# Optimization experiments

Measured on AMD Instinct MI355X. Metric: run time of the kernel, lower is better.

Reference implementation:

```python
import jax, jax.numpy as jnp
import numpy as np

N_HEADS = 8
HEAD_CH = 64
NC = N_HEADS * HEAD_CH  # 512
SCALE = HEAD_CH ** -0.5


def _grid_sample_bilinear(img, grid):
    # img [N,C,H,W]; grid [N,Hg,Wg,2] as (x,y) in [-1,1]; align_corners=True, zeros padding
    N, C, H, W = img.shape
    gx, gy = grid[..., 0], grid[..., 1]
    ix = (gx + 1.0) * 0.5 * (W - 1)
    iy = (gy + 1.0) * 0.5 * (H - 1)
    ix0 = jnp.floor(ix)
    iy0 = jnp.floor(iy)
    ix1 = ix0 + 1.0
    iy1 = iy0 + 1.0
    flat = img.reshape(N, C, H * W)

    def gather(yy, xx):
        yi = jnp.clip(yy, 0, H - 1).astype(jnp.int32)
        xi = jnp.clip(xx, 0, W - 1).astype(jnp.int32)
        idx = (yi * W + xi).reshape(N, 1, -1)
        v = jnp.take_along_axis(flat, idx, axis=2)  # [N,C,Hg*Wg]
        m = ((yy >= 0) & (yy <= H - 1) & (xx >= 0) & (xx <= W - 1)).astype(img.dtype)
        return v * m.reshape(N, 1, -1)

    w00 = ((ix1 - ix) * (iy1 - iy)).reshape(N, 1, -1)
    w01 = ((ix - ix0) * (iy1 - iy)).reshape(N, 1, -1)
    w10 = ((ix1 - ix) * (iy - iy0)).reshape(N, 1, -1)
    w11 = ((ix - ix0) * (iy - iy0)).reshape(N, 1, -1)
    out = (gather(iy0, ix0) * w00 + gather(iy0, ix1) * w01 +
           gather(iy1, ix0) * w10 + gather(iy1, ix1) * w11)
    return out.reshape(N, C, grid.shape[1], grid.shape[2])


def _attn_single(qv, xv, w_q, b_q, w_k, b_k, w_v, b_v, w_o, b_o):
    # qv [Bx,C] single query; xv [Bx,C,L] keys/values; batched forward_attn_single
    Bx, L = qv.shape[0], xv.shape[2]
    qh = (qv @ w_q.T + b_q).reshape(Bx, N_HEADS, HEAD_CH)
    k = (jnp.einsum('oc,bcl->bol', w_k, xv) + b_k[None, :, None]).reshape(Bx, N_HEADS, HEAD_CH, L)
    v = (jnp.einsum('oc,bcl->bol', w_v, xv) + b_v[None, :, None]).reshape(Bx, N_HEADS, HEAD_CH, L)
    a = jax.nn.softmax(jnp.einsum('bhc,bhcl->bhl', qh, k) * SCALE, axis=-1)
    o = jnp.einsum('bhl,bhcl->bhc', a, v).reshape(Bx, NC)
    return o @ w_o.T + b_o


def _forward(q, x, w_off_proj, b_off_proj, w_dw, b_dw, ln_g, ln_b, w_off,
             w_q, b_q, w_k, b_k, w_v, b_v, w_o, b_o, H, W):
    B, NQ, C = q.shape
    x_img = x.transpose(0, 2, 1).reshape(B, C, H, W)
    # proj_offset (1x1 conv)
    t = jnp.einsum('oc,bchw->bohw', w_off_proj, x_img) + b_off_proj[None, :, None, None]
    # depthwise 3x3 conv (groups = channels), stride 1, pad 1
    t = jax.lax.conv_general_dilated(
        t, w_dw, (1, 1), ((1, 1), (1, 1)), feature_group_count=C,
        dimension_numbers=('NCHW', 'OIHW', 'NCHW')) + b_dw[None, :, None, None]
    # LayerNormProxy: LN over channel dim
    tc = t.transpose(0, 2, 3, 1)
    mu = tc.mean(-1, keepdims=True)
    var = tc.var(-1, keepdims=True)
    tc = (tc - mu) / jnp.sqrt(var + 1e-5) * ln_g + ln_b
    t = jax.nn.gelu(tc.transpose(0, 3, 1, 2), approximate=False)
    # 1x1 conv -> 2 offset channels (y, x), no bias
    offset = jnp.einsum('oc,bchw->bohw', w_off, t)
    Hk, Wk = offset.shape[2], offset.shape[3]
    offset = offset.transpose(0, 2, 3, 1)  # [B,Hk,Wk,2]
    ry = (jnp.linspace(0.5, Hk - 0.5, Hk, dtype=x.dtype) / Hk) * 2 - 1
    rx = (jnp.linspace(0.5, Wk - 0.5, Wk, dtype=x.dtype) / Wk) * 2 - 1
    ref = jnp.stack(jnp.meshgrid(ry, rx, indexing='ij'), axis=-1)  # [Hk,Wk,2] (y,x)
    pos = jnp.tanh(offset + ref)  # offset_range_factor=None branch
    xs = _grid_sample_bilinear(x_img, pos[..., ::-1])  # grid as (x,y) -> [B,C,Hk,Wk]
    ap = (w_q, b_q, w_k, b_k, w_v, b_v, w_o, b_o)
    # ra_type='gar': first query attends over all samples
    y0 = _attn_single(q[:, 0], xs.reshape(B, C, Hk * Wk), *ap)
    # remaining queries each attend over a 2-row chunk of samples (vectorized over chunks)
    nchunk = Hk // 2
    xc = xs.reshape(B, C, nchunk, 2, Wk).transpose(0, 2, 1, 3, 4).reshape(B * nchunk, C, 2 * Wk)
    qc = q[:, 1:1 + nchunk].reshape(B * nchunk, C)
    yc = _attn_single(qc, xc, *ap).reshape(B, nchunk, C)
    return jnp.concatenate([y0[:, None, :], yc], axis=1)  # [B, NQ, C]


def setup_inputs() -> dict:
    key = jax.random.key(0)
    ks = jax.random.split(key, 9)
    B, NQ, C, H, W = 16, 33, 512, 64, 64
    f32 = jnp.float32
    return {
        'q': jax.random.normal(ks[0], (B, NQ, C), f32),
        'x': jax.random.normal(ks[1], (B, H * W, C), f32),
        'w_off_proj': jax.random.normal(ks[2], (C, C), f32) * 0.02,
        'b_off_proj': jnp.zeros((C,), f32),
        'w_dw': jax.random.normal(ks[3], (C, 1, 3, 3), f32) * 0.02,
        'b_dw': jnp.zeros((C,), f32),
        'ln_g': jnp.ones((C,), f32),
        'ln_b': jnp.zeros((C,), f32),
        'w_off': jax.random.normal(ks[4], (2, C), f32) * 0.02,
        'w_q': jax.random.normal(ks[5], (C, C), f32) * 0.02,
        'b_q': jnp.zeros((C,), f32),
        'w_k': jax.random.normal(ks[6], (C, C), f32) * 0.02,
        'b_k': jnp.zeros((C,), f32),
        'w_v': jax.random.normal(ks[7], (C, C), f32) * 0.02,
        'b_v': jnp.zeros((C,), f32),
        'w_o': jax.random.normal(ks[8], (C, C), f32) * 0.02,
        'b_o': jnp.zeros((C,), f32),
        'H': H,
        'W': W,
    }


def reference(q, x, w_off_proj, b_off_proj, w_dw, b_dw, ln_g, ln_b, w_off,
              w_q, b_q, w_k, b_k, w_v, b_v, w_o, b_o, H, W):
    return _forward(q, x, w_off_proj, b_off_proj, w_dw, b_dw, ln_g, ln_b, w_off,
                    w_q, b_q, w_k, b_k, w_v, b_v, w_o, b_o, H, W)
```

## Files before the change

### kernel.cpp

```cpp
#include <hip/hip_runtime.h>
#include <hip/hip_bf16.h>

#define CDIM 512
#define HWSZ 4096
#define BATCH 16
#define NQTOT 33

typedef short bf16x8 __attribute__((ext_vector_type(8)));
typedef float f32x4 __attribute__((ext_vector_type(4)));

__device__ __forceinline__ unsigned short f2bf(float f) {
  unsigned int u = __float_as_uint(f);
  u += 0x7fffu + ((u >> 16) & 1u);
  return (unsigned short)(u >> 16);
}
__device__ __forceinline__ float bf2f(unsigned short s) {
  return __uint_as_float((unsigned int)s << 16);
}
__device__ __forceinline__ void gload16(const void* g, void* l) {
  __builtin_amdgcn_global_load_lds((const __attribute__((address_space(1))) void*)g,
                                   (__attribute__((address_space(3))) void*)l, 16, 0, 0);
}
__device__ __forceinline__ float fast_erf(float x) {
  float ax = fabsf(x);
  float t = __builtin_amdgcn_rcpf(fmaf(0.3275911f, ax, 1.f));
  float p = fmaf(t, 1.061405429f, -1.453152027f);
  p = fmaf(t, p, 1.421413741f);
  p = fmaf(t, p, -0.284496736f);
  p = fmaf(t, p, 0.254829592f);
  p = p * t;
  float e = 1.f - p * __expf(-ax * ax);
  return copysignf(e, x);
}
__device__ __forceinline__ float gelu(float x) {
  return x * 0.5f * (1.f + fast_erf(x * 0.70710678118654752f));
}
__device__ __forceinline__ int2 swz_tiles(int nwgx) {
  int nwg = gridDim.x * gridDim.y;
  int l = blockIdx.y * gridDim.x + blockIdx.x;
  int w = (l & 7) * (nwg >> 3) + (l >> 3);
  return make_int2((w % nwgx) * 128, (w / nwgx) * 128);
}

#define SBM 64
#define SBN 64
#define SBK 16

__global__ __launch_bounds__(256) void gemm_sm_nt(const float* __restrict__ A,
                                                  const float* __restrict__ Wt,
                                                  const float* __restrict__ bias,
                                                  float* __restrict__ C, int M) {
  const int K = CDIM, N = CDIM;
  __shared__ float As[SBK][SBM + 4];
  __shared__ float Bs[SBK][SBN + 4];
  int tid = threadIdx.x;
  int n0 = blockIdx.x * SBN;
  int m0 = blockIdx.y * SBM;
  int ty = tid >> 4, tx = tid & 15;
  float acc[4][4];
#pragma unroll
  for (int i = 0; i < 4; ++i)
#pragma unroll
    for (int j = 0; j < 4; ++j) acc[i][j] = 0.f;

  int lrow = tid >> 2, lkk = (tid & 3) << 2;
  for (int k0 = 0; k0 < K; k0 += SBK) {
    float4 va = make_float4(0.f, 0.f, 0.f, 0.f);
    if (m0 + lrow < M) va = *(const float4*)(A + (size_t)(m0 + lrow) * K + k0 + lkk);
    As[lkk + 0][lrow] = va.x; As[lkk + 1][lrow] = va.y;
    As[lkk + 2][lrow] = va.z; As[lkk + 3][lrow] = va.w;
    float4 vb = *(const float4*)(Wt + (size_t)(n0 + lrow) * K + k0 + lkk);
    Bs[lkk + 0][lrow] = vb.x; Bs[lkk + 1][lrow] = vb.y;
    Bs[lkk + 2][lrow] = vb.z; Bs[lkk + 3][lrow] = vb.w;
    __syncthreads();
#pragma unroll
    for (int k = 0; k < SBK; ++k) {
      float a[4], b[4];
      *(float4*)&a[0] = *(float4*)&As[k][ty * 4];
      *(float4*)&b[0] = *(float4*)&Bs[k][tx * 4];
#pragma unroll
      for (int i = 0; i < 4; ++i)
#pragma unroll
        for (int j = 0; j < 4; ++j) acc[i][j] = fmaf(a[i], b[j], acc[i][j]);
    }
    __syncthreads();
  }
#pragma unroll
  for (int i = 0; i < 4; ++i) {
    int m = m0 + ty * 4 + i;
    if (m >= M) continue;
    int n = n0 + tx * 4;
    float4 v;
    v.x = acc[i][0] + bias[n + 0];
    v.y = acc[i][1] + bias[n + 1];
    v.z = acc[i][2] + bias[n + 2];
    v.w = acc[i][3] + bias[n + 3];
    *(float4*)(C + (size_t)m * N + n) = v;
  }
}

__global__ __launch_bounds__(256) void gemm_kv_nt(const unsigned short* __restrict__ A,
                                                  const unsigned short* __restrict__ Wkv,
                                                  const float* __restrict__ bk,
                                                  const float* __restrict__ bv,
                                                  unsigned short* __restrict__ K,
                                                  unsigned short* __restrict__ V) {
  __shared__ unsigned short As[128 * 32];
  __shared__ unsigned short Ws[128 * 32];
  int tid = threadIdx.x;
  int wave = tid >> 6, lane = tid & 63;
  int2 t = swz_tiles(gridDim.x);
  int n0 = t.x, m0 = t.y;
  int wm = (wave >> 1) * 64, wn = (wave & 1) * 64;
  f32x4 acc[4][4];
#pragma unroll
  for (int i = 0; i < 4; ++i)
#pragma unroll
    for (int j = 0; j < 4; ++j) acc[i][j] = (f32x4){0.f, 0.f, 0.f, 0.f};

  int rsel = lane & 15;
  int ksel = (lane >> 4) * 8;

  for (int k0 = 0; k0 < CDIM; k0 += 32) {
#pragma unroll
    for (int c = 0; c < 2; ++c) {
      int s = c * 256 + tid;
      int row = s >> 2, ch = s & 3;
      gload16(A + (size_t)(m0 + row) * CDIM + k0 + ch * 8, (void*)(As + (size_t)s * 8));
      gload16(Wkv + (size_t)(n0 + row) * CDIM + k0 + ch * 8, (void*)(Ws + (size_t)s * 8));
    }
    __syncthreads();
    bf16x8 af[4], bfr[4];
#pragma unroll
    for (int mf = 0; mf < 4; ++mf)
      af[mf] = *(const bf16x8*)&As[(wm + mf * 16 + rsel) * 32 + ksel];
#pragma unroll
    for (int nf = 0; nf < 4; ++nf)
      bfr[nf] = *(const bf16x8*)&Ws[(wn + nf * 16 + rsel) * 32 + ksel];
#pragma unroll
    for (int mf = 0; mf < 4; ++mf)
#pragma unroll
      for (int nf = 0; nf < 4; ++nf)
        acc[mf][nf] = __builtin_amdgcn_mfma_f32_16x16x32_bf16(af[mf], bfr[nf], acc[mf][nf], 0, 0, 0);
    __syncthreads();
  }
  const float* bias = (n0 < 512) ? bk : bv;
  unsigned short* C = (n0 < 512) ? K : V;
  int nb = (n0 < 512) ? n0 : n0 - 512;
#pragma unroll
  for (int nf = 0; nf < 4; ++nf) {
    int col = nb + wn + nf * 16 + (lane & 15);
    float bv2 = bias[col];
#pragma unroll
    for (int mf = 0; mf < 4; ++mf) {
      int rbase = m0 + wm + mf * 16 + (lane >> 4) * 4;
#pragma unroll
      for (int i = 0; i < 4; ++i)
        C[(size_t)(rbase + i) * CDIM + col] = f2bf(acc[mf][nf][i] + bv2);
    }
  }
}

__global__ __launch_bounds__(256) void gemm3_nt(const float* __restrict__ A,
                                                const unsigned short* __restrict__ Whi,
                                                const unsigned short* __restrict__ Wlo,
                                                const float* __restrict__ bias,
                                                float* __restrict__ C) {
  __shared__ unsigned short AsH[128 * 64];
  __shared__ unsigned short AsL[128 * 64];
  __shared__ unsigned short WsH[128 * 64];
  __shared__ unsigned short WsL[128 * 64];
  int tid = threadIdx.x;
  int wave = tid >> 6, lane = tid & 63;
  int2 t = swz_tiles(gridDim.x);
  int n0 = t.x, m0 = t.y;
  int wm = (wave >> 1) * 64, wn = (wave & 1) * 64;
  f32x4 acc[4][4];
#pragma unroll
  for (int i = 0; i < 4; ++i)
#pragma unroll
    for (int j = 0; j < 4; ++j) acc[i][j] = (f32x4){0.f, 0.f, 0.f, 0.f};

  int rsel = lane & 15;
  int kcsel = lane >> 4;

  float4 ar0[4], ar1[4];
#pragma unroll
  for (int c = 0; c < 4; ++c) {
    int s = c * 256 + tid;
    int row = s >> 3, qc = s & 7;
    const float4* src = (const float4*)(A + (size_t)(m0 + row) * CDIM + (size_t)(qc ^ (row & 7)) * 8);
    ar0[c] = src[0];
    ar1[c] = src[1];
  }

  for (int k0 = 0; k0 < CDIM; k0 += 64) {
#pragma unroll
    for (int c = 0; c < 4; ++c) {
      int s = c * 256 + tid;
      int row = s >> 3, ch = s & 7;
      size_t gw = (size_t)(n0 + row) * CDIM + k0 + (size_t)(ch ^ (row & 7)) * 8;
      gload16(Whi + gw, (void*)(WsH + (size_t)s * 8));
      gload16(Wlo + gw, (void*)(WsL + (size_t)s * 8));
    }
#pragma unroll
    for (int c = 0; c < 4; ++c) {
      int s = c * 256 + tid;
      float vv[8] = {ar0[c].x, ar0[c].y, ar0[c].z, ar0[c].w,
                     ar1[c].x, ar1[c].y, ar1[c].z, ar1[c].w};
      unsigned int hw[4], lw[4];
#pragma unroll
      for (int j = 0; j < 4; ++j) {
        unsigned int u0 = __float_as_uint(vv[2 * j]);
        unsigned int u1 = __float_as_uint(vv[2 * j + 1]);
        hw[j] = (u0 >> 16) | (u1 & 0xffff0000u);
        float l0 = vv[2 * j] - __uint_as_float(u0 & 0xffff0000u);
        float l1 = vv[2 * j + 1] - __uint_as_float(u1 & 0xffff0000u);
        __hip_bfloat162 l2 = __float22bfloat162_rn(make_float2(l0, l1));
        lw[j] = *reinterpret_cast<unsigned int*>(&l2);
      }
      *(uint4*)&AsH[(size_t)s * 8] = make_uint4(hw[0], hw[1], hw[2], hw[3]);
      *(uint4*)&AsL[(size_t)s * 8] = make_uint4(lw[0], lw[1], lw[2], lw[3]);
    }
    __syncthreads();
    if (k0 + 64 < CDIM) {
#pragma unroll
      for (int c = 0; c < 4; ++c) {
        int s = c * 256 + tid;
        int row = s >> 3, qc = s & 7;
        const float4* src = (const float4*)(A + (size_t)(m0 + row) * CDIM + (k0 + 64) + (size_t)(qc ^ (row & 7)) * 8);
        ar0[c] = src[0];
        ar1[c] = src[1];
      }
    }
#pragma unroll
    for (int half = 0; half < 2; ++half) {
      int cb = half * 4 + kcsel;
      bf16x8 ah[4], al[4], bh[4], bl[4];
#pragma unroll
      for (int mf = 0; mf < 4; ++mf) {
        int row = wm + mf * 16 + rsel;
        int off = (row * 8 + (cb ^ (row & 7))) * 8;
        ah[mf] = *(const bf16x8*)&AsH[off];
        al[mf] = *(const bf16x8*)&AsL[off];
      }
#pragma unroll
      for (int nf = 0; nf < 4; ++nf) {
        int row = wn + nf * 16 + rsel;
        int off = (row * 8 + (cb ^ (row & 7))) * 8;
        bh[nf] = *(const bf16x8*)&WsH[off];
        bl[nf] = *(const bf16x8*)&WsL[off];
      }
#pragma unroll
      for (int mf = 0; mf < 4; ++mf)
#pragma unroll
        for (int nf = 0; nf < 4; ++nf) {
          acc[mf][nf] = __builtin_amdgcn_mfma_f32_16x16x32_bf16(ah[mf], bh[nf], acc[mf][nf], 0, 0, 0);
          acc[mf][nf] = __builtin_amdgcn_mfma_f32_16x16x32_bf16(ah[mf], bl[nf], acc[mf][nf], 0, 0, 0);
          acc[mf][nf] = __builtin_amdgcn_mfma_f32_16x16x32_bf16(al[mf], bh[nf], acc[mf][nf], 0, 0, 0);
        }
    }
    __syncthreads();
  }
#pragma unroll
  for (int nf = 0; nf < 4; ++nf) {
    int col = n0 + wn + nf * 16 + (lane & 15);
    float bvs = bias[col];
#pragma unroll
    for (int mf = 0; mf < 4; ++mf) {
      int rbase = m0 + wm + mf * 16 + (lane >> 4) * 4;
#pragma unroll
      for (int i = 0; i < 4; ++i)
        C[(size_t)(rbase + i) * CDIM + col] = acc[mf][nf][i] + bvs;
    }
  }
}

__global__ __launch_bounds__(256) void conv_all(const float* __restrict__ w_off_proj,
                                                const float* __restrict__ w_k,
                                                const float* __restrict__ w_v,
                                                const float* __restrict__ w_dw,
                                                unsigned short* __restrict__ wphi,
                                                unsigned short* __restrict__ wplo,
                                                unsigned short* __restrict__ wkv,
                                                float* __restrict__ wdwT) {
  int blk = blockIdx.x, tid = threadIdx.x;
  if (blk < 256) {
    int i = blk * 256 + tid;
    float4 v = ((const float4*)w_off_proj)[i];
    ushort4 h, l;
    h.x = f2bf(v.x); l.x = f2bf(v.x - bf2f(h.x));
    h.y = f2bf(v.y); l.y = f2bf(v.y - bf2f(h.y));
    h.z = f2bf(v.z); l.z = f2bf(v.z - bf2f(h.z));
    h.w = f2bf(v.w); l.w = f2bf(v.w - bf2f(h.w));
    ((ushort4*)wphi)[i] = h;
    ((ushort4*)wplo)[i] = l;
  } else if (blk < 512) {
    int i = (blk - 256) * 256 + tid;
    float4 v = ((const float4*)w_k)[i];
    ushort4 o;
    o.x = f2bf(v.x); o.y = f2bf(v.y); o.z = f2bf(v.z); o.w = f2bf(v.w);
    ((ushort4*)wkv)[i] = o;
  } else if (blk < 768) {
    int i = (blk - 512) * 256 + tid;
    float4 v = ((const float4*)w_v)[i];
    ushort4 o;
    o.x = f2bf(v.x); o.y = f2bf(v.y); o.z = f2bf(v.z); o.w = f2bf(v.w);
    ((ushort4*)(wkv + (size_t)CDIM * CDIM))[i] = o;
  } else {
    int id = (blk - 768) * 256 + tid;
    if (id < 9 * CDIM) wdwT[id] = w_dw[(id & 511) * 9 + (id >> 9)];
  }
}

__global__ __launch_bounds__(512) void offset_gather_kernel(
    const float* __restrict__ t0, const float* __restrict__ x,
    const float* __restrict__ w_dwT, const float* __restrict__ b_dw,
    const float* __restrict__ ln_g, const float* __restrict__ ln_b,
    const float* __restrict__ w_off, unsigned short* __restrict__ xs) {
  __shared__ float4 sten[30 * 128];

  int blk = blockIdx.x;
  int b = blk >> 9, rem = blk & 511;
  int h = rem >> 3, w0 = (rem & 7) << 3;
  int t = threadIdx.x;
  const float* base = t0 + (size_t)b * HWSZ * CDIM;

  for (int s = t; s < 30 * 128; s += 512) {
    int ps = s >> 7, q = s & 127;
    int r = ps / 10, cs = ps - r * 10;
    int hh = h + r - 1, ww = w0 + cs - 1;
    if ((unsigned)hh < 64u && (unsigned)ww < 64u) {
      gload16(base + (size_t)(hh * 64 + ww) * CDIM + 4 * q, (void*)(sten + s));
    } else {
      sten[s] = make_float4(0.f, 0.f, 0.f, 0.f);
    }
  }
  __syncthreads();

  int w = t >> 6;
  int lane = t & 63;
  float4 acc0 = ((const float4*)b_dw)[lane];
  float4 acc1 = ((const float4*)b_dw)[64 + lane];
#pragma unroll
  for (int r = 0; r < 3; ++r)
#pragma unroll
    for (int dxi = 0; dxi < 3; ++dxi) {
      const float4* wrow = (const float4*)(w_dwT + (size_t)(r * 3 + dxi) * CDIM);
      float4 w40 = wrow[lane], w41 = wrow[64 + lane];
      int pt = (r * 10 + w + dxi) * 128;
      float4 v0 = sten[pt + lane];
      float4 v1 = sten[pt + 64 + lane];
      acc0.x = fmaf(v0.x, w40.x, acc0.x);
      acc0.y = fmaf(v0.y, w40.y, acc0.y);
      acc0.z = fmaf(v0.z, w40.z, acc0.z);
      acc0.w = fmaf(v0.w, w40.w, acc0.w);
      acc1.x = fmaf(v1.x, w41.x, acc1.x);
      acc1.y = fmaf(v1.y, w41.y, acc1.y);
      acc1.z = fmaf(v1.z, w41.z, acc1.z);
      acc1.w = fmaf(v1.w, w41.w, acc1.w);
    }
  float s1 = acc0.x + acc0.y + acc0.z + acc0.w + acc1.x + acc1.y + acc1.z + acc1.w;
  float s2 = acc0.x * acc0.x + acc0.y * acc0.y + acc0.z * acc0.z + acc0.w * acc0.w +
             acc1.x * acc1.x + acc1.y * acc1.y + acc1.z * acc1.z + acc1.w * acc1.w;
#pragma unroll
  for (int off = 32; off; off >>= 1) {
    s1 += __shfl_xor(s1, off, 64);
    s2 += __shfl_xor(s2, off, 64);
  }
  float mean = s1 * (1.f / 512.f);
  float var = s2 * (1.f / 512.f) - mean * mean;
  float inv = 1.f / sqrtf(var + 1e-5f);

  float4 g0 = ((const float4*)ln_g)[lane], g1 = ((const float4*)ln_g)[64 + lane];
  float4 lb0 = ((const float4*)ln_b)[lane], lb1 = ((const float4*)ln_b)[64 + lane];
  float4 wy0 = ((const float4*)w_off)[lane], wy1 = ((const float4*)w_off)[64 + lane];
  float4 wx0 = ((const float4*)(w_off + CDIM))[lane], wx1 = ((const float4*)(w_off + CDIM))[64 + lane];
  float4 ge0, ge1;
  ge0.x = gelu((acc0.x - mean) * inv * g0.x + lb0.x);
  ge0.y = gelu((acc0.y - mean) * inv * g0.y + lb0.y);
  ge0.z = gelu((acc0.z - mean) * inv * g0.z + lb0.z);
  ge0.w = gelu((acc0.w - mean) * inv * g0.w + lb0.w);
  ge1.x = gelu((acc1.x - mean) * inv * g1.x + lb1.x);
  ge1.y = gelu((acc1.y - mean) * inv * g1.y + lb1.y);
  ge1.z = gelu((acc1.z - mean) * inv * g1.z + lb1.z);
  ge1.w = gelu((acc1.w - mean) * inv * g1.w + lb1.w);
  float oy = ge0.x * wy0.x + ge0.y * wy0.y + ge0.z * wy0.z + ge0.w * wy0.w +
             ge1.x * wy1.x + ge1.y * wy1.y + ge1.z * wy1.z + ge1.w * wy1.w;
  float ox = ge0.x * wx0.x + ge0.y * wx0.y + ge0.z * wx0.z + ge0.w * wx0.w +
             ge1.x * wx1.x + ge1.y * wx1.y + ge1.z * wx1.z + ge1.w * wx1.w;
#pragma unroll
  for (int off = 32; off; off >>= 1) {
    oy += __shfl_xor(oy, off, 64);
    ox += __shfl_xor(ox, off, 64);
  }
  int wcol = w0 + w;
  float ry = ((float)h + 0.5f) / 64.f * 2.f - 1.f;
  float rx = ((float)wcol + 0.5f) / 64.f * 2.f - 1.f;
  float py = tanhf(oy + ry);
  float px = tanhf(ox + rx);
  float fx = (px + 1.f) * 0.5f * 63.f;
  float fy = (py + 1.f) * 0.5f * 63.f;
  float fx0 = floorf(fx), fy0 = floorf(fy);
  float fx1 = fx0 + 1.f, fy1 = fy0 + 1.f;
  float wx1f = fx - fx0, wx0f = fx1 - fx;
  float wy1f = fy - fy0, wy0f = fy1 - fy;
  float m00 = (fy0 >= 0.f && fy0 <= 63.f && fx0 >= 0.f && fx0 <= 63.f) ? 1.f : 0.f;
  float m01 = (fy0 >= 0.f && fy0 <= 63.f && fx1 >= 0.f && fx1 <= 63.f) ? 1.f : 0.f;
  float m10 = (fy1 >= 0.f && fy1 <= 63.f && fx0 >= 0.f && fx0 <= 63.f) ? 1.f : 0.f;
  float m11 = (fy1 >= 0.f && fy1 <= 63.f && fx1 >= 0.f && fx1 <= 63.f) ? 1.f : 0.f;
  int xi0 = min(max((int)fx0, 0), 63), xi1 = min(max((int)fx1, 0), 63);
  int yi0 = min(max((int)fy0, 0), 63), yi1 = min(max((int)fy1, 0), 63);
  int i00 = yi0 * 64 + xi0, i01 = yi0 * 64 + xi1;
  int i10 = yi1 * 64 + xi0, i11 = yi1 * 64 + xi1;
  float wtx = wx0f * wy0f * m00, wty = wx1f * wy0f * m01;
  float wtz = wx0f * wy1f * m10, wtw = wx1f * wy1f * m11;

  const float* xb = x + (size_t)b * HWSZ * CDIM;
  float4 A0 = ((const float4*)(xb + (size_t)i00 * CDIM))[lane];
  float4 A1 = ((const float4*)(xb + (size_t)i00 * CDIM))[64 + lane];
  float4 B0 = ((const float4*)(xb + (size_t)i01 * CDIM))[lane];
  float4 B1 = ((const float4*)(xb + (size_t)i01 * CDIM))[64 + lane];
  float4 C0 = ((const float4*)(xb + (size_t)i10 * CDIM))[lane];
  float4 C1 = ((const float4*)(xb + (size_t)i10 * CDIM))[64 + lane];
  float4 D0 = ((const float4*)(xb + (size_t)i11 * CDIM))[lane];
  float4 D1 = ((const float4*)(xb + (size_t)i11 * CDIM))[64 + lane];
  ushort4 o0, o1;
  o0.x = f2bf(A0.x * wtx + B0.x * wty + C0.x * wtz + D0.x * wtw);
  o0.y = f2bf(A0.y * wtx + B0.y * wty + C0.y * wtz + D0.y * wtw);
  o0.z = f2bf(A0.z * wtx + B0.z * wty + C0.z * wtz + D0.z * wtw);
  o0.w = f2bf(A0.w * wtx + B0.w * wty + C0.w * wtz + D0.w * wtw);
  o1.x = f2bf(A1.x * wtx + B1.x * wty + C1.x * wtz + D1.x * wtw);
  o1.y = f2bf(A1.y * wtx + B1.y * wty + C1.y * wtz + D1.y * wtw);
  o1.z = f2bf(A1.z * wtx + B1.z * wty + C1.z * wtz + D1.z * wtw);
  o1.w = f2bf(A1.w * wtx + B1.w * wty + C1.w * wtz + D1.w * wtw);
  size_t posg = (size_t)b * HWSZ + h * 64 + wcol;
  *(ushort4*)(xs + posg * CDIM + 4 * lane) = o0;
  *(ushort4*)(xs + posg * CDIM + 256 + 4 * lane) = o1;
}

__global__ __launch_bounds__(256) void attn_split_kernel(const float* __restrict__ qh,
                                                         const unsigned short* __restrict__ kk,
                                                         const unsigned short* __restrict__ vv,
                                                         float* __restrict__ pm,
                                                         float* __restrict__ ps,
                                                         float* __restrict__ po) {
  __shared__ float sc0[128], sc1[128];
  __shared__ float qs0[64], qs1[64];
  __shared__ float red0[4], red1[4];
  __shared__ float part0[4][64], part1[4][64];
  int bid = blockIdx.x;
  int h = bid & 7;
  int bs = bid >> 3;
  int b = bs >> 5, s = bs & 31;
  int l0 = s << 7;
  int task0 = b * 33;
  int task1 = b * 33 + s + 1;
  int tid = threadIdx.x;
  if (tid < 64) qs0[tid] = qh[(size_t)task0 * CDIM + h * 64 + tid];
  else if (tid < 128) qs1[tid - 64] = qh[(size_t)task1 * CDIM + h * 64 + (tid - 64)];
  __syncthreads();

  const unsigned short* kb = kk + ((size_t)b * HWSZ + l0) * CDIM + h * 64;
  float lmax0 = -INFINITY, lmax1 = -INFINITY;
  if (tid < 128) {
    const uint4* kr = (const uint4*)(kb + (size_t)tid * CDIM);
    float sv0 = 0.f, sv1 = 0.f;
#pragma unroll
    for (int c = 0; c < 8; ++c) {
      uint4 kv = kr[c];
      float k0 = __uint_as_float(kv.x << 16);
      float k1 = __uint_as_float(kv.x & 0xffff0000u);
      float k2 = __uint_as_float(kv.y << 16);
      float k3 = __uint_as_float(kv.y & 0xffff0000u);
      float k4 = __uint_as_float(kv.z << 16);
      float k5 = __uint_as_float(kv.z & 0xffff0000u);
      float k6 = __uint_as_float(kv.w << 16);
      float k7 = __uint_as_float(kv.w & 0xffff0000u);
      sv0 = fmaf(k0, qs0[8 * c + 0], sv0); sv1 = fmaf(k0, qs1[8 * c + 0], sv1);
      sv0 = fmaf(k1, qs0[8 * c + 1], sv0); sv1 = fmaf(k1, qs1[8 * c + 1], sv1);
      sv0 = fmaf(k2, qs0[8 * c + 2], sv0); sv1 = fmaf(k2, qs1[8 * c + 2], sv1);
      sv0 = fmaf(k3, qs0[8 * c + 3], sv0); sv1 = fmaf(k3, qs1[8 * c + 3], sv1);
      sv0 = fmaf(k4, qs0[8 * c + 4], sv0); sv1 = fmaf(k4, qs1[8 * c + 4], sv1);
      sv0 = fmaf(k5, qs0[8 * c + 5], sv0); sv1 = fmaf(k5, qs1[8 * c + 5], sv1);
      sv0 = fmaf(k6, qs0[8 * c + 6], sv0); sv1 = fmaf(k6, qs1[8 * c + 6], sv1);
      sv0 = fmaf(k7, qs0[8 * c + 7], sv0); sv1 = fmaf(k7, qs1[8 * c + 7], sv1);
    }
    sv0 *= 0.125f; sv1 *= 0.125f;
    sc0[tid] = sv0; sc1[tid] = sv1;
    lmax0 = sv0; lmax1 = sv1;
  }
#pragma unroll
  for (int off = 32; off; off >>= 1) {
    lmax0 = fmaxf(lmax0, __shfl_xor(lmax0, off, 64));
    lmax1 = fmaxf(lmax1, __shfl_xor(lmax1, off, 64));
  }
  if (!(tid & 63)) { red0[tid >> 6] = lmax0; red1[tid >> 6] = lmax1; }
  __syncthreads();
  lmax0 = fmaxf(fmaxf(red0[0], red0[1]), fmaxf(red0[2], red0[3]));
  lmax1 = fmaxf(fmaxf(red1[0], red1[1]), fmaxf(red1[2], red1[3]));
  __syncthreads();

  float ls0 = 0.f, ls1 = 0.f;
  if (tid < 128) {
    float e0 = expf(sc0[tid] - lmax0);
    float e1 = expf(sc1[tid] - lmax1);
    sc0[tid] = e0; sc1[tid] = e1;
    ls0 = e0; ls1 = e1;
  }
#pragma unroll
  for (int off = 32; off; off >>= 1) {
    ls0 += __shfl_xor(ls0, off, 64);
    ls1 += __shfl_xor(ls1, off, 64);
  }
  if (!(tid & 63)) { red0[tid >> 6] = ls0; red1[tid >> 6] = ls1; }
  __syncthreads();
  float tsum0 = red0[0] + red0[1] + red0[2] + red0[3];
  float tsum1 = red1[0] + red1[1] + red1[2] + red1[3];

  int ch = tid & 63, g = tid >> 6;
  const unsigned short* vb = vv + ((size_t)b * HWSZ + l0) * CDIM + h * 64 + ch;
  float o0 = 0.f, o1 = 0.f;
#pragma unroll 4
  for (int l = g; l < 128; l += 4) {
    float vvv = bf2f(vb[(size_t)l * CDIM]);
    o0 = fmaf(sc0[l], vvv, o0);
    o1 = fmaf(sc1[l], vvv, o1);
  }
  part0[g][ch] = o0;
  part1[g][ch] = o1;
  __syncthreads();
  if (tid < 64) {
    float r0 = part0[0][tid] + part0[1][tid] + part0[2][tid] + part0[3][tid];
    float r1 = part1[0][tid] + part1[1][tid] + part1[2][tid] + part1[3][tid];
    int bid0 = (b * 64 + s) * 8 + h;
    int bid1 = (b * 64 + 32 + s) * 8 + h;
    po[(size_t)bid0 * 64 + tid] = r0;
    po[(size_t)bid1 * 64 + tid] = r1;
    if (tid == 0) {
      pm[bid0] = lmax0; ps[bid0] = tsum0;
      pm[bid1] = lmax1; ps[bid1] = tsum1;
    }
  }
}

__global__ __launch_bounds__(64) void attn_reduce_kernel(const float* __restrict__ pm,
                                                         const float* __restrict__ ps,
                                                         const float* __restrict__ po,
                                                         float* __restrict__ oo) {
  int bid = blockIdx.x;
  int h = bid & 7, task = bid >> 3;
  int b = task / 33, qidx = task - b * 33;
  int sbase = (qidx == 0) ? 0 : 31 + qidx;
  int ns = (qidx == 0) ? 32 : 1;
  int t = threadIdx.x;
  float mg = -INFINITY;
  for (int i = 0; i < ns; ++i) mg = fmaxf(mg, pm[((size_t)(b * 64 + sbase + i)) * 8 + h]);
  float tot = 0.f, o = 0.f;
  for (int i = 0; i < ns; ++i) {
    size_t pi = ((size_t)(b * 64 + sbase + i)) * 8 + h;
    float w = expf(pm[pi] - mg);
    tot = fmaf(ps[pi], w, tot);
    o = fmaf(po[pi * 64 + t], w, o);
  }
  oo[(size_t)task * CDIM + h * 64 + t] = o / tot;
}

extern "C" void kernel_launch(void* const* d_in, const int* in_sizes, int n_in,
                              void* d_out, int out_size, void* d_ws, size_t ws_size,
                              hipStream_t stream) {
  const float* q          = (const float*)d_in[0];
  const float* x          = (const float*)d_in[1];
  const float* w_off_proj = (const float*)d_in[2];
  const float* b_off_proj = (const float*)d_in[3];
  const float* w_dw       = (const float*)d_in[4];
  const float* b_dw       = (const float*)d_in[5];
  const float* ln_g       = (const float*)d_in[6];
  const float* ln_b       = (const float*)d_in[7];
  const float* w_off      = (const float*)d_in[8];
  const float* w_q        = (const float*)d_in[9];
  const float* b_q        = (const float*)d_in[10];
  const float* w_k        = (const float*)d_in[11];
  const float* b_k        = (const float*)d_in[12];
  const float* w_v        = (const float*)d_in[13];
  const float* b_v        = (const float*)d_in[14];
  const float* w_o        = (const float*)d_in[15];
  const float* b_o        = (const float*)d_in[16];

  char* ws = (char*)d_ws;
  size_t off = 0;
  const size_t NBIG = (size_t)BATCH * HWSZ * CDIM;
  const int NSPLIT = BATCH * 64 * 8;
  float* t0    = (float*)(ws + off);                  off += NBIG * 4;
  unsigned short* xs_bf = (unsigned short*)(ws + off); off += NBIG * 2;
  unsigned short* k_bf  = (unsigned short*)(ws + off); off += NBIG * 2;
  unsigned short* v_bf  = (unsigned short*)(ws + off); off += NBIG * 2;
  unsigned short* wphi = (unsigned short*)(ws + off);  off += (size_t)CDIM * CDIM * 2;
  unsigned short* wplo = (unsigned short*)(ws + off);  off += (size_t)CDIM * CDIM * 2;
  unsigned short* wkv_bf = (unsigned short*)(ws + off); off += (size_t)2 * CDIM * CDIM * 2;
  float* w_dwT = (float*)(ws + off);                  off += (size_t)9 * CDIM * 4;
  float* qh    = (float*)(ws + off);                  off += (size_t)BATCH * NQTOT * CDIM * 4;
  float* o_all = (float*)(ws + off);                  off += (size_t)BATCH * NQTOT * CDIM * 4;
  float* pm    = (float*)(ws + off);                  off += (size_t)NSPLIT * 4;
  float* ps    = (float*)(ws + off);                  off += (size_t)NSPLIT * 4;
  float* po    = (float*)(ws + off);                  off += (size_t)NSPLIT * 64 * 4;

  const int Mbig = BATCH * HWSZ;
  const int Msm  = BATCH * NQTOT;
  dim3 gSm2(CDIM / SBN, (Msm + SBM - 1) / SBM);
  dim3 gMf(CDIM / 128, Mbig / 128);
  dim3 gKV(2 * CDIM / 128, Mbig / 128);

  conv_all<<<786, 256, 0, stream>>>(w_off_proj, w_k, w_v, w_dw, wphi, wplo, wkv_bf, w_dwT);
  gemm3_nt<<<gMf, 256, 0, stream>>>(x, wphi, wplo, b_off_proj, t0);
  offset_gather_kernel<<<Mbig / 8, 512, 0, stream>>>(t0, x, w_dwT, b_dw, ln_g, ln_b, w_off, xs_bf);
  gemm_kv_nt<<<gKV, 256, 0, stream>>>(xs_bf, wkv_bf, b_k, b_v, k_bf, v_bf);
  gemm_sm_nt<<<gSm2, 256, 0, stream>>>(q, w_q, b_q, qh, Msm);
  attn_split_kernel<<<NSPLIT / 2, 256, 0, stream>>>(qh, k_bf, v_bf, pm, ps, po);
  attn_reduce_kernel<<<Msm * 8, 64, 0, stream>>>(pm, ps, po, o_all);
  gemm_sm_nt<<<gSm2, 256, 0, stream>>>(o_all, w_o, b_o, (float*)d_out, Msm);
}
```

Before: 459.2 us.

## Double-buffer gemm3_nt LDS tiles with BK=32 and single barrier per step

Restructures the split-bf16 3-MFMA GEMM main loop to use two LDS buffers of K=32 slices instead of one K=64 buffer. The next slice's A and W loads are issued before the current slice's MFMAs, and the hi/lo split is written into the alternate buffer afterwards, leaving one barrier per iteration. It uses manual waitcnt and setprio around the MFMA block. This aims to overlap global loads with compute and cut barrier stalls, at the cost of twice as many loop iterations and hand-tuned vmcnt counts that must match the load order exactly.

After: 502.7 us. +9.5%, slower.

```diff
diff --git a/kernel.cpp b/kernel.cpp
--- a/kernel.cpp
+++ b/kernel.cpp
@@ -166,10 +166,10 @@
                                                 const unsigned short* __restrict__ Wlo,
                                                 const float* __restrict__ bias,
                                                 float* __restrict__ C) {
-  __shared__ unsigned short AsH[128 * 64];
-  __shared__ unsigned short AsL[128 * 64];
-  __shared__ unsigned short WsH[128 * 64];
-  __shared__ unsigned short WsL[128 * 64];
+  __shared__ unsigned short AsH[2][128 * 32];
+  __shared__ unsigned short AsL[2][128 * 32];
+  __shared__ unsigned short WsH[2][128 * 32];
+  __shared__ unsigned short WsL[2][128 * 32];
   int tid = threadIdx.x;
   int wave = tid >> 6, lane = tid & 63;
   int2 t = swz_tiles(gridDim.x);
@@ -184,84 +184,101 @@
   int rsel = lane & 15;
   int kcsel = lane >> 4;
 
-  float4 ar0[4], ar1[4];
-#pragma unroll
-  for (int c = 0; c < 4; ++c) {
-    int s = c * 256 + tid;
-    int row = s >> 3, qc = s & 7;
-    const float4* src = (const float4*)(A + (size_t)(m0 + row) * CDIM + (size_t)(qc ^ (row & 7)) * 8);
-    ar0[c] = src[0];
-    ar1[c] = src[1];
-  }
-
-  for (int k0 = 0; k0 < CDIM; k0 += 64) {
-#pragma unroll
-    for (int c = 0; c < 4; ++c) {
-      int s = c * 256 + tid;
-      int row = s >> 3, ch = s & 7;
-      size_t gw = (size_t)(n0 + row) * CDIM + k0 + (size_t)(ch ^ (row & 7)) * 8;
-      gload16(Whi + gw, (void*)(WsH + (size_t)s * 8));
-      gload16(Wlo + gw, (void*)(WsL + (size_t)s * 8));
-    }
-#pragma unroll
-    for (int c = 0; c < 4; ++c) {
-      int s = c * 256 + tid;
-      float vv[8] = {ar0[c].x, ar0[c].y, ar0[c].z, ar0[c].w,
-                     ar1[c].x, ar1[c].y, ar1[c].z, ar1[c].w};
-      unsigned int hw[4], lw[4];
-#pragma unroll
-      for (int j = 0; j < 4; ++j) {
-        unsigned int u0 = __float_as_uint(vv[2 * j]);
-        unsigned int u1 = __float_as_uint(vv[2 * j + 1]);
-        hw[j] = (u0 >> 16) | (u1 & 0xffff0000u);
-        float l0 = vv[2 * j] - __uint_as_float(u0 & 0xffff0000u);
-        float l1 = vv[2 * j + 1] - __uint_as_float(u1 & 0xffff0000u);
-        __hip_bfloat162 l2 = __float22bfloat162_rn(make_float2(l0, l1));
-        lw[j] = *reinterpret_cast<unsigned int*>(&l2);
+  int s0 = tid, s1 = 256 + tid;
+  int row0 = s0 >> 2, gch0 = (s0 & 3) ^ (row0 & 3);
+  int row1 = s1 >> 2, gch1 = (s1 & 3) ^ (row1 & 3);
+  const float* arow0 = A + (size_t)(m0 + row0) * CDIM + gch0 * 8;
+  const float* arow1 = A + (size_t)(m0 + row1) * CDIM + gch1 * 8;
+  const unsigned short* whrow0 = Whi + (size_t)(n0 + row0) * CDIM + gch0 * 8;
+  const unsigned short* wlrow0 = Wlo + (size_t)(n0 + row0) * CDIM + gch0 * 8;
+  const unsigned short* whrow1 = Whi + (size_t)(n0 + row1) * CDIM + gch1 * 8;
+  const unsigned short* wlrow1 = Wlo + (size_t)(n0 + row1) * CDIM + gch1 * 8;
+
+  float4 a00, a01, a10, a11;
+
+#define SPLIT_WRITE(BUF, V0, V1, SLOT)                                         \
+  {                                                                            \
+    float vv[8] = {(V0).x, (V0).y, (V0).z, (V0).w,                             \
+                   (V1).x, (V1).y, (V1).z, (V1).w};                            \
+    unsigned int hw[4], lw[4];                                                 \
+    _Pragma("unroll")                                                          \
+    for (int j = 0; j < 4; ++j) {                                              \
+      unsigned int u0 = __float_as_uint(vv[2 * j]);                            \
+      unsigned int u1 = __float_as_uint(vv[2 * j + 1]);                        \
+      hw[j] = (u0 >> 16) | (u1 & 0xffff0000u);                                 \
+      float l0 = vv[2 * j] - __uint_as_float(u0 & 0xffff0000u);                \
+      float l1 = vv[2 * j + 1] - __uint_as_float(u1 & 0xffff0000u);            \
+      __hip_bfloat162 l2 = __float22bfloat162_rn(make_float2(l0, l1));         \
+      lw[j] = *reinterpret_cast<unsigned int*>(&l2);                           \
+    }                                                                          \
+    *(uint4*)&AsH[BUF][(size_t)(SLOT)*8] = make_uint4(hw[0], hw[1], hw[2], hw[3]); \
+    *(uint4*)&AsL[BUF][(size_t)(SLOT)*8] = make_uint4(lw[0], lw[1], lw[2], lw[3]); \
+  }
+
+  a00 = ((const float4*)arow0)[0]; a01 = ((const float4*)arow0)[1];
+  a10 = ((const float4*)arow1)[0]; a11 = ((const float4*)arow1)[1];
+  gload16(whrow0, (void*)(WsH[0] + (size_t)s0 * 8));
+  gload16(wlrow0, (void*)(WsL[0] + (size_t)s0 * 8));
+  gload16(whrow1, (void*)(WsH[0] + (size_t)s1 * 8));
+  gload16(wlrow1, (void*)(WsL[0] + (size_t)s1 * 8));
+  asm volatile("s_waitcnt vmcnt(0)" ::: "memory");
+  SPLIT_WRITE(0, a00, a01, s0);
+  SPLIT_WRITE(0, a10, a11, s1);
+  asm volatile("s_waitcnt lgkmcnt(0)" ::: "memory");
+  __builtin_amdgcn_s_barrier();
+  asm volatile("" ::: "memory");
+
+  int cur = 0;
+  for (int tt = 0; tt < 16; ++tt) {
+    if (tt < 15) {
+      int kn = (tt + 1) * 32;
+      a00 = ((const float4*)(arow0 + kn))[0]; a01 = ((const float4*)(arow0 + kn))[1];
+      a10 = ((const float4*)(arow1 + kn))[0]; a11 = ((const float4*)(arow1 + kn))[1];
+      int nx = cur ^ 1;
+      gload16(whrow0 + kn, (void*)(WsH[nx] + (size_t)s0 * 8));
+      gload16(wlrow0 + kn, (void*)(WsL[nx] + (size_t)s0 * 8));
+      gload16(whrow1 + kn, (void*)(WsH[nx] + (size_t)s1 * 8));
+      gload16(wlrow1 + kn, (void*)(WsL[nx] + (size_t)s1 * 8));
+      asm volatile("s_waitcnt vmcnt(8)" ::: "memory");
+    } else {
+      asm volatile("s_waitcnt vmcnt(0)" ::: "memory");
+    }
+    __builtin_amdgcn_s_setprio(1);
+    bf16x8 ah[4], al[4], bh[4], bl[4];
+#pragma unroll
+    for (int mf = 0; mf < 4; ++mf) {
+      int row = wm + mf * 16 + rsel;
+      int off = ((row << 2) + (kcsel ^ (row & 3))) * 8;
+      ah[mf] = *(const bf16x8*)&AsH[cur][off];
+      al[mf] = *(const bf16x8*)&AsL[cur][off];
+    }
+#pragma unroll
+    for (int nf = 0; nf < 4; ++nf) {
+      int row = wn + nf * 16 + rsel;
+      int off = ((row << 2) + (kcsel ^ (row & 3))) * 8;
+      bh[nf] = *(const bf16x8*)&WsH[cur][off];
+      bl[nf] = *(const bf16x8*)&WsL[cur][off];
+    }
+#pragma unroll
+    for (int mf = 0; mf < 4; ++mf)
+#pragma unroll
+      for (int nf = 0; nf < 4; ++nf) {
+        acc[mf][nf] = __builtin_amdgcn_mfma_f32_16x16x32_bf16(ah[mf], bh[nf], acc[mf][nf], 0, 0, 0);
+        acc[mf][nf] = __builtin_amdgcn_mfma_f32_16x16x32_bf16(ah[mf], bl[nf], acc[mf][nf], 0, 0, 0);
+        acc[mf][nf] = __builtin_amdgcn_mfma_f32_16x16x32_bf16(al[mf], bh[nf], acc[mf][nf], 0, 0, 0);
       }
-      *(uint4*)&AsH[(size_t)s * 8] = make_uint4(hw[0], hw[1], hw[2], hw[3]);
-      *(uint4*)&AsL[(size_t)s * 8] = make_uint4(lw[0], lw[1], lw[2], lw[3]);
-    }
-    __syncthreads();
-    if (k0 + 64 < CDIM) {
-#pragma unroll
-      for (int c = 0; c < 4; ++c) {
-        int s = c * 256 + tid;
-        int row = s >> 3, qc = s & 7;
-        const float4* src = (const float4*)(A + (size_t)(m0 + row) * CDIM + (k0 + 64) + (size_t)(qc ^ (row & 7)) * 8);
-        ar0[c] = src[0];
-        ar1[c] = src[1];
-      }
-    }
-#pragma unroll
-    for (int half = 0; half < 2; ++half) {
-      int cb = half * 4 + kcsel;
-      bf16x8 ah[4], al[4], bh[4], bl[4];
-#pragma unroll
-      for (int mf = 0; mf < 4; ++mf) {
-        int row = wm + mf * 16 + rsel;
-        int off = (row * 8 + (cb ^ (row & 7))) * 8;
-        ah[mf] = *(const bf16x8*)&AsH[off];
-        al[mf] = *(const bf16x8*)&AsL[off];
-      }
-#pragma unroll
-      for (int nf = 0; nf < 4; ++nf) {
-        int row = wn + nf * 16 + rsel;
-        int off = (row * 8 + (cb ^ (row & 7))) * 8;
-        bh[nf] = *(const bf16x8*)&WsH[off];
-        bl[nf] = *(const bf16x8*)&WsL[off];
-      }
-#pragma unroll
-      for (int mf = 0; mf < 4; ++mf)
-#pragma unroll
-        for (int nf = 0; nf < 4; ++nf) {
-          acc[mf][nf] = __builtin_amdgcn_mfma_f32_16x16x32_bf16(ah[mf], bh[nf], acc[mf][nf], 0, 0, 0);
-          acc[mf][nf] = __builtin_amdgcn_mfma_f32_16x16x32_bf16(ah[mf], bl[nf], acc[mf][nf], 0, 0, 0);
-          acc[mf][nf] = __builtin_amdgcn_mfma_f32_16x16x32_bf16(al[mf], bh[nf], acc[mf][nf], 0, 0, 0);
-        }
-    }
-    __syncthreads();
-  }
+    __builtin_amdgcn_s_setprio(0);
+    if (tt < 15) {
+      SPLIT_WRITE(cur ^ 1, a00, a01, s0);
+      SPLIT_WRITE(cur ^ 1, a10, a11, s1);
+      asm volatile("s_waitcnt lgkmcnt(0)" ::: "memory");
+      __builtin_amdgcn_s_barrier();
+      asm volatile("" ::: "memory");
+      cur ^= 1;
+    }
+  }
+#undef SPLIT_WRITE
+
 #pragma unroll
   for (int nf = 0; nf < 4; ++nf) {
     int col = n0 + wn + nf * 16 + (lane & 15);
```
